# Performance work log

Measured on AMD Instinct MI355X. Metric: run time of the kernel, lower is better.

The kernel has to match this reference:

```python
import jax, jax.numpy as jnp
import numpy as np

T, H, I, E = 2048, 2880, 2880, 8
TOP_K = 4
ALPHA = 1.702   # hidden_act_alpha
LIMIT = 7.0     # swiglu_limit
BETA = 1.0      # swiglu_beta


def setup_inputs() -> dict:
    key = jax.random.key(0)
    ks = jax.random.split(key, 10)
    s = 0.02
    return {
        "hidden_states": jax.random.normal(ks[0], (T, H), dtype=jnp.float32),
        "w_router": jax.random.normal(ks[1], (E, H), dtype=jnp.float32) * s,
        "b_router": jax.random.normal(ks[2], (E,), dtype=jnp.float32) * s,
        "w_gate": jax.random.normal(ks[3], (E, I, H), dtype=jnp.float32) * s,
        "b_gate": jax.random.normal(ks[4], (E, I), dtype=jnp.float32) * s,
        "w_up": jax.random.normal(ks[5], (E, I, H), dtype=jnp.float32) * s,
        "b_up": jax.random.normal(ks[6], (E, I), dtype=jnp.float32) * s,
        "w2": jax.random.normal(ks[7], (E, H, I), dtype=jnp.float32) * s,
        "b2": jax.random.normal(ks[8], (E, H), dtype=jnp.float32) * s,
        "num_global_tokens": T,
        "max_num_tokens_per_gpu": T,
    }


def reference(hidden_states, w_router, b_router, w_gate, b_gate, w_up, b_up,
              w2, b2, num_global_tokens, max_num_tokens_per_gpu):
    x = hidden_states  # [T, H]
    # ---- router + custom routing_function: topk then softmax over topk logits (fp32)
    router_logits = x @ w_router.T + b_router                 # [T, E]
    topk_vals, topk_idx = jax.lax.top_k(router_logits, TOP_K)  # [T, K]
    expert_weights = jax.nn.softmax(topk_vals.astype(jnp.float32), axis=-1)  # [T, K]
    # combine weights per expert: [T, E], nonzero only for the top-k experts
    tok = jnp.arange(x.shape[0])[:, None]
    combine = jnp.zeros((x.shape[0], E), dtype=jnp.float32).at[tok, topk_idx].add(expert_weights)
    # ---- experts: gpt-oss swiglu with clamp limits and +beta on up branch
    g = jnp.einsum('th,eih->tei', x, w_gate) + b_gate[None]   # [T, E, I]
    u = jnp.einsum('th,eih->tei', x, w_up) + b_up[None]       # [T, E, I]
    g = jnp.minimum(g, LIMIT)
    u = jnp.clip(u, -LIMIT, LIMIT)
    act = (u + BETA) * (g * jax.nn.sigmoid(ALPHA * g))        # [T, E, I]
    y = jnp.einsum('tei,ehi->teh', act, w2) + b2[None]        # [T, E, H]
    out = jnp.einsum('teh,te->th', y, combine)                # [T, H]
    return out.astype(x.dtype)
```

## Files before the change

### kernel.cpp

```cpp
#include <hip/hip_runtime.h>
#include <hip/hip_bf16.h>
#include <cstdint>

#define T_TOK 2048
#define HD    2880
#define ID    2880
#define NE    8
#define TOPK  4
#define ALPHA 1.702f
#define LIMIT 7.0f

typedef __attribute__((ext_vector_type(8))) short short8;
typedef __attribute__((ext_vector_type(4))) float floatx4;

__device__ __forceinline__ ushort f32_bf16(float f) {
    union { float f; uint32_t u; } c; c.f = f;
    uint32_t u = c.u;
    uint32_t r = (u + 0x7FFFu + ((u >> 16) & 1u)) >> 16;
    return (ushort)r;
}

__global__ __launch_bounds__(256) void cvt_x_kernel(const float* __restrict__ x,
                                                    ushort* __restrict__ xb) {
    int i = (blockIdx.x * 256 + threadIdx.x) * 4;
    float4 v = *(const float4*)(x + i);
    ushort4 o;
    o.x = f32_bf16(v.x); o.y = f32_bf16(v.y);
    o.z = f32_bf16(v.z); o.w = f32_bf16(v.w);
    *(ushort4*)(xb + i) = o;
}

__global__ __launch_bounds__(256) void router_kernel(
    const float* __restrict__ x, const float* __restrict__ wr,
    const float* __restrict__ br, int* __restrict__ cnt,
    int* __restrict__ tok_list, float* __restrict__ wgt_list) {
    const int t = blockIdx.x, tid = threadIdx.x;
    __shared__ float sx[HD];
    __shared__ float sred[NE][4];
    for (int h = tid; h < HD; h += 256) sx[h] = x[(size_t)t * HD + h];
    __syncthreads();
    float p[NE];
#pragma unroll
    for (int e = 0; e < NE; e++) p[e] = 0.f;
    for (int h = tid; h < HD; h += 256) {
        float xv = sx[h];
#pragma unroll
        for (int e = 0; e < NE; e++) p[e] = fmaf(xv, wr[e * HD + h], p[e]);
    }
#pragma unroll
    for (int e = 0; e < NE; e++) {
#pragma unroll
        for (int off = 32; off > 0; off >>= 1) p[e] += __shfl_down(p[e], off, 64);
    }
    if ((tid & 63) == 0) {
#pragma unroll
        for (int e = 0; e < NE; e++) sred[e][tid >> 6] = p[e];
    }
    __syncthreads();
    if (tid == 0) {
        float lg[NE];
#pragma unroll
        for (int e = 0; e < NE; e++)
            lg[e] = sred[e][0] + sred[e][1] + sred[e][2] + sred[e][3] + br[e];
        int idx[TOPK]; float val[TOPK];
        unsigned used = 0;
#pragma unroll
        for (int k = 0; k < TOPK; k++) {
            int best = -1; float bv = -1e30f;
#pragma unroll
            for (int e = 0; e < NE; e++) {
                if (!((used >> e) & 1u) && lg[e] > bv) { bv = lg[e]; best = e; }
            }
            used |= 1u << best; idx[k] = best; val[k] = bv;
        }
        float m = val[0];
        float ex[TOPK], s = 0.f;
#pragma unroll
        for (int k = 0; k < TOPK; k++) { ex[k] = __expf(val[k] - m); s += ex[k]; }
        float inv = 1.f / s;
#pragma unroll
        for (int k = 0; k < TOPK; k++) {
            int e = idx[k];
            int pos = atomicAdd(&cnt[e], 1);
            tok_list[e * T_TOK + pos] = t;
            wgt_list[e * T_TOK + pos] = ex[k] * inv;
        }
    }
}

__global__ void offsets_kernel(const int* __restrict__ cnt, int* __restrict__ ofs) {
    if (threadIdx.x == 0 && blockIdx.x == 0) {
        int s = 0;
        for (int e = 0; e < NE; e++) { ofs[e] = s; s += cnt[e]; }
    }
}

#define LDS_S 40
__global__ __launch_bounds__(256, 2) void expert_gu_kernel(
    const ushort* __restrict__ xb, const float* __restrict__ wg,
    const float* __restrict__ bg, const float* __restrict__ wu,
    const float* __restrict__ bu, const int* __restrict__ cnt,
    const int* __restrict__ ofs, const int* __restrict__ tok_list,
    ushort* __restrict__ act) {
    const int e = blockIdx.z;
    const int n_e = cnt[e];
    const int mBase = blockIdx.y * 128;
    if (mBase >= n_e) return;
    const int nBase = blockIdx.x * 128;
    const int tid = threadIdx.x;

    __shared__ ushort sA[128 * LDS_S];
    __shared__ ushort sBg[128 * LDS_S];
    __shared__ ushort sBu[128 * LDS_S];
    __shared__ int sTok[128];

    if (tid < 128) {
        int slot = mBase + tid;
        sTok[tid] = tok_list[e * T_TOK + (slot < n_e ? slot : 0)];
    }
    __syncthreads();

    const int wave = tid >> 6, lane = tid & 63;
    const int wm = (wave >> 1) * 64, wn = (wave & 1) * 64;
    const int ln = lane & 15, quad = lane >> 4;

    floatx4 accG[4][4], accU[4][4];
#pragma unroll
    for (int mi = 0; mi < 4; mi++)
#pragma unroll
        for (int ni = 0; ni < 4; ni++) {
            accG[mi][ni] = (floatx4){0.f, 0.f, 0.f, 0.f};
            accU[mi][ni] = (floatx4){0.f, 0.f, 0.f, 0.f};
        }

    const float* wgE = wg + (size_t)e * ID * HD;
    const float* wuE = wu + (size_t)e * ID * HD;

    for (int k0 = 0; k0 < HD; k0 += 32) {
#pragma unroll
        for (int r = 0; r < 2; r++) {
            int lin = r * 256 + tid;
            int ar = lin >> 2, ac = lin & 3;
            uint4 v = *(const uint4*)(xb + (size_t)sTok[ar] * HD + k0 + ac * 8);
            *(uint4*)&sA[ar * LDS_S + ac * 8] = v;
        }
#pragma unroll
        for (int r = 0; r < 4; r++) {
            int c = r * 256 + tid;
            int brow = c >> 3, bc = c & 7;
            int n = nBase + brow; if (n >= ID) n = ID - 1;
            float4 g4 = *(const float4*)(wgE + (size_t)n * HD + k0 + bc * 4);
            float4 u4 = *(const float4*)(wuE + (size_t)n * HD + k0 + bc * 4);
            ushort4 gg, uu;
            gg.x = f32_bf16(g4.x); gg.y = f32_bf16(g4.y);
            gg.z = f32_bf16(g4.z); gg.w = f32_bf16(g4.w);
            uu.x = f32_bf16(u4.x); uu.y = f32_bf16(u4.y);
            uu.z = f32_bf16(u4.z); uu.w = f32_bf16(u4.w);
            *(ushort4*)&sBg[brow * LDS_S + bc * 4] = gg;
            *(ushort4*)&sBu[brow * LDS_S + bc * 4] = uu;
        }
        __syncthreads();
        short8 af[4], bgf[4], buf_[4];
#pragma unroll
        for (int mi = 0; mi < 4; mi++)
            af[mi] = *(const short8*)&sA[(wm + mi * 16 + ln) * LDS_S + quad * 8];
#pragma unroll
        for (int ni = 0; ni < 4; ni++) {
            bgf[ni] = *(const short8*)&sBg[(wn + ni * 16 + ln) * LDS_S + quad * 8];
            buf_[ni] = *(const short8*)&sBu[(wn + ni * 16 + ln) * LDS_S + quad * 8];
        }
#pragma unroll
        for (int mi = 0; mi < 4; mi++)
#pragma unroll
            for (int ni = 0; ni < 4; ni++) {
                accG[mi][ni] = __builtin_amdgcn_mfma_f32_16x16x32_bf16(
                    af[mi], bgf[ni], accG[mi][ni], 0, 0, 0);
                accU[mi][ni] = __builtin_amdgcn_mfma_f32_16x16x32_bf16(
                    af[mi], buf_[ni], accU[mi][ni], 0, 0, 0);
            }
        __syncthreads();
    }

    const int row0 = ofs[e] + mBase;
#pragma unroll
    for (int mi = 0; mi < 4; mi++) {
#pragma unroll
        for (int r = 0; r < 4; r++) {
            int ml = wm + mi * 16 + quad * 4 + r;
            if (mBase + ml >= n_e) continue;
#pragma unroll
            for (int ni = 0; ni < 4; ni++) {
                int n = nBase + wn + ni * 16 + ln;
                if (n < ID) {
                    float g = accG[mi][ni][r] + bg[e * ID + n];
                    float u = accU[mi][ni][r] + bu[e * ID + n];
                    g = fminf(g, LIMIT);
                    u = fminf(fmaxf(u, -LIMIT), LIMIT);
                    float sg = 1.0f / (1.0f + __expf(-ALPHA * g));
                    float a = (u + 1.0f) * (g * sg);
                    act[(size_t)(row0 + ml) * ID + n] = f32_bf16(a);
                }
            }
        }
    }
}

__global__ __launch_bounds__(256, 2) void expert_down_kernel(
    const ushort* __restrict__ act, const float* __restrict__ w2,
    const float* __restrict__ b2, const int* __restrict__ cnt,
    const int* __restrict__ ofs, const int* __restrict__ tok_list,
    const float* __restrict__ wgt_list, float* __restrict__ out) {
    const int e = blockIdx.z;
    const int n_e = cnt[e];
    const int mBase = blockIdx.y * 128;
    if (mBase >= n_e) return;
    const int nBase = blockIdx.x * 128;
    const int tid = threadIdx.x;

    __shared__ ushort sA[128 * LDS_S];
    __shared__ ushort sB[128 * LDS_S];
    __shared__ int sTok[128];
    __shared__ float sWgt[128];

    if (tid < 128) {
        int slot = mBase + tid;
        int cs = (slot < n_e) ? slot : 0;
        sTok[tid] = tok_list[e * T_TOK + cs];
        sWgt[tid] = wgt_list[e * T_TOK + cs];
    }
    __syncthreads();

    const int wave = tid >> 6, lane = tid & 63;
    const int wm = (wave >> 1) * 64, wn = (wave & 1) * 64;
    const int ln = lane & 15, quad = lane >> 4;
    const int row0 = ofs[e] + mBase;

    floatx4 acc[4][4];
#pragma unroll
    for (int mi = 0; mi < 4; mi++)
#pragma unroll
        for (int ni = 0; ni < 4; ni++) acc[mi][ni] = (floatx4){0.f, 0.f, 0.f, 0.f};

    const float* w2E = w2 + (size_t)e * HD * ID;

    for (int k0 = 0; k0 < ID; k0 += 32) {
#pragma unroll
        for (int r = 0; r < 2; r++) {
            int lin = r * 256 + tid;
            int ar = lin >> 2, ac = lin & 3;
            int rr = (mBase + ar < n_e) ? ar : 0;
            uint4 v = *(const uint4*)(act + (size_t)(row0 + rr) * ID + k0 + ac * 8);
            *(uint4*)&sA[ar * LDS_S + ac * 8] = v;
        }
#pragma unroll
        for (int r = 0; r < 4; r++) {
            int c = r * 256 + tid;
            int brow = c >> 3, bc = c & 7;
            int n = nBase + brow; if (n >= HD) n = HD - 1;
            float4 b4 = *(const float4*)(w2E + (size_t)n * ID + k0 + bc * 4);
            ushort4 bb;
            bb.x = f32_bf16(b4.x); bb.y = f32_bf16(b4.y);
            bb.z = f32_bf16(b4.z); bb.w = f32_bf16(b4.w);
            *(ushort4*)&sB[brow * LDS_S + bc * 4] = bb;
        }
        __syncthreads();
        short8 af[4], bf[4];
#pragma unroll
        for (int mi = 0; mi < 4; mi++)
            af[mi] = *(const short8*)&sA[(wm + mi * 16 + ln) * LDS_S + quad * 8];
#pragma unroll
        for (int ni = 0; ni < 4; ni++)
            bf[ni] = *(const short8*)&sB[(wn + ni * 16 + ln) * LDS_S + quad * 8];
#pragma unroll
        for (int mi = 0; mi < 4; mi++)
#pragma unroll
            for (int ni = 0; ni < 4; ni++)
                acc[mi][ni] = __builtin_amdgcn_mfma_f32_16x16x32_bf16(
                    af[mi], bf[ni], acc[mi][ni], 0, 0, 0);
        __syncthreads();
    }

#pragma unroll
    for (int mi = 0; mi < 4; mi++) {
#pragma unroll
        for (int r = 0; r < 4; r++) {
            int ml = wm + mi * 16 + quad * 4 + r;
            if (mBase + ml >= n_e) continue;
            int token = sTok[ml];
            float wgt = sWgt[ml];
#pragma unroll
            for (int ni = 0; ni < 4; ni++) {
                int n = nBase + wn + ni * 16 + ln;
                if (n < HD) {
                    float v = (acc[mi][ni][r] + b2[e * HD + n]) * wgt;
                    atomicAdd(&out[(size_t)token * HD + n], v);
                }
            }
        }
    }
}

extern "C" void kernel_launch(void* const* d_in, const int* in_sizes, int n_in,
                              void* d_out, int out_size, void* d_ws, size_t ws_size,
                              hipStream_t stream) {
    const float* x  = (const float*)d_in[0];
    const float* wr = (const float*)d_in[1];
    const float* br = (const float*)d_in[2];
    const float* wg = (const float*)d_in[3];
    const float* bg = (const float*)d_in[4];
    const float* wu = (const float*)d_in[5];
    const float* bu = (const float*)d_in[6];
    const float* w2 = (const float*)d_in[7];
    const float* b2 = (const float*)d_in[8];
    float* out = (float*)d_out;

    char* ws = (char*)d_ws;
    int*    cnt      = (int*)ws;
    int*    ofs      = (int*)(ws + 256);
    int*    tok_list = (int*)(ws + 512);
    float*  wgt_list = (float*)(ws + 512 + 65536);
    ushort* xb       = (ushort*)(ws + 512 + 131072);
    ushort* act      = (ushort*)(ws + 512 + 131072 + 11796480);

    hipMemsetAsync(out, 0, (size_t)T_TOK * HD * sizeof(float), stream);
    hipMemsetAsync(cnt, 0, NE * sizeof(int), stream);

    cvt_x_kernel<<<(T_TOK * HD) / 4 / 256, 256, 0, stream>>>(x, xb);
    router_kernel<<<T_TOK, 256, 0, stream>>>(x, wr, br, cnt, tok_list, wgt_list);
    offsets_kernel<<<1, 64, 0, stream>>>(cnt, ofs);

    dim3 g1((ID + 127) / 128, T_TOK / 128, NE);
    expert_gu_kernel<<<g1, 256, 0, stream>>>(xb, wg, bg, wu, bu, cnt, ofs, tok_list, act);

    dim3 g2((HD + 127) / 128, T_TOK / 128, NE);
    expert_down_kernel<<<g2, 256, 0, stream>>>(act, w2, b2, cnt, ofs, tok_list, wgt_list, out);
}
```

Baseline: 1.847 ms.

## Pre-convert expert weights to bf16 and stream tiles via global_load_lds

```diff
diff --git a/kernel.cpp b/kernel.cpp
--- a/kernel.cpp
+++ b/kernel.cpp
@@ -1,6 +1,6 @@
 #include <hip/hip_runtime.h>
-#include <hip/hip_bf16.h>
 #include <cstdint>
+#include <cstddef>
 
 #define T_TOK 2048
 #define HD    2880
@@ -18,6 +18,13 @@
     uint32_t u = c.u;
     uint32_t r = (u + 0x7FFFu + ((u >> 16) & 1u)) >> 16;
     return (ushort)r;
+}
+
+__device__ __forceinline__ void gload_lds16(const void* g, void* l) {
+    __builtin_amdgcn_global_load_lds(
+        (const __attribute__((address_space(1))) void*)g,
+        (__attribute__((address_space(3))) void*)l,
+        16, 0, 0);
 }
 
 __global__ __launch_bounds__(256) void cvt_x_kernel(const float* __restrict__ x,
@@ -28,6 +35,18 @@
     o.x = f32_bf16(v.x); o.y = f32_bf16(v.y);
     o.z = f32_bf16(v.z); o.w = f32_bf16(v.w);
     *(ushort4*)(xb + i) = o;
+}
+
+__global__ __launch_bounds__(256) void cvt_w_kernel(const float* __restrict__ w,
+                                                    ushort* __restrict__ wb, int n4) {
+    int stride = gridDim.x * 256;
+    for (int i = blockIdx.x * 256 + threadIdx.x; i < n4; i += stride) {
+        float4 v = *(const float4*)(w + (size_t)i * 4);
+        ushort4 o;
+        o.x = f32_bf16(v.x); o.y = f32_bf16(v.y);
+        o.z = f32_bf16(v.z); o.w = f32_bf16(v.w);
+        *(ushort4*)(wb + (size_t)i * 4) = o;
+    }
 }
 
 __global__ __launch_bounds__(256) void router_kernel(
@@ -92,6 +111,208 @@
     if (threadIdx.x == 0 && blockIdx.x == 0) {
         int s = 0;
         for (int e = 0; e < NE; e++) { ofs[e] = s; s += cnt[e]; }
+    }
+}
+
+
+__global__ __launch_bounds__(256, 2) void expert_gu2_kernel(
+    const ushort* __restrict__ xb, const ushort* __restrict__ wgb,
+    const float* __restrict__ bg, const ushort* __restrict__ wub,
+    const float* __restrict__ bu, const int* __restrict__ cnt,
+    const int* __restrict__ ofs, const int* __restrict__ tok_list,
+    ushort* __restrict__ act) {
+    const int e = blockIdx.z;
+    const int n_e = cnt[e];
+    const int mBase = blockIdx.y * 128;
+    if (mBase >= n_e) return;
+    const int nBase = blockIdx.x * 128;
+    const int tid = threadIdx.x;
+
+    __shared__ __attribute__((aligned(16))) ushort sA[128 * 32];
+    __shared__ __attribute__((aligned(16))) ushort sBg[128 * 32];
+    __shared__ __attribute__((aligned(16))) ushort sBu[128 * 32];
+    __shared__ int sTok[128];
+
+    if (tid < 128) {
+        int slot = mBase + tid;
+        sTok[tid] = tok_list[e * T_TOK + (slot < n_e ? slot : 0)];
+    }
+    __syncthreads();
+
+    const ushort* wgE = wgb + (size_t)e * (size_t)ID * HD;
+    const ushort* wuE = wub + (size_t)e * (size_t)ID * HD;
+    const ushort* aSrc[2];
+    const ushort* gSrc[2];
+    const ushort* uSrc[2];
+#pragma unroll
+    for (int i = 0; i < 2; i++) {
+        int lin = i * 256 + tid;
+        int ar = lin >> 2, ac = lin & 3;
+        aSrc[i] = xb + (size_t)sTok[ar] * HD + ac * 8;
+        int n = nBase + ar; if (n >= ID) n = ID - 1;
+        gSrc[i] = wgE + (size_t)n * HD + ac * 8;
+        uSrc[i] = wuE + (size_t)n * HD + ac * 8;
+    }
+
+    const int wave = tid >> 6, lane = tid & 63;
+    const int wm = (wave >> 1) * 64, wn = (wave & 1) * 64;
+    const int ln = lane & 15, quad = lane >> 4;
+
+    floatx4 accG[4][4], accU[4][4];
+#pragma unroll
+    for (int mi = 0; mi < 4; mi++)
+#pragma unroll
+        for (int ni = 0; ni < 4; ni++) {
+            accG[mi][ni] = (floatx4){0.f, 0.f, 0.f, 0.f};
+            accU[mi][ni] = (floatx4){0.f, 0.f, 0.f, 0.f};
+        }
+
+    for (int k0 = 0; k0 < HD; k0 += 32) {
+#pragma unroll
+        for (int i = 0; i < 2; i++) {
+            int lin = i * 256 + tid;
+            gload_lds16(aSrc[i] + k0, &sA[lin * 8]);
+            gload_lds16(gSrc[i] + k0, &sBg[lin * 8]);
+            gload_lds16(uSrc[i] + k0, &sBu[lin * 8]);
+        }
+        __syncthreads();
+
+        short8 af[4], bgf[4], buf_[4];
+#pragma unroll
+        for (int mi = 0; mi < 4; mi++)
+            af[mi] = *(const short8*)&sA[(wm + mi * 16 + ln) * 32 + quad * 8];
+#pragma unroll
+        for (int ni = 0; ni < 4; ni++) {
+            bgf[ni] = *(const short8*)&sBg[(wn + ni * 16 + ln) * 32 + quad * 8];
+            buf_[ni] = *(const short8*)&sBu[(wn + ni * 16 + ln) * 32 + quad * 8];
+        }
+#pragma unroll
+        for (int mi = 0; mi < 4; mi++)
+#pragma unroll
+            for (int ni = 0; ni < 4; ni++) {
+                accG[mi][ni] = __builtin_amdgcn_mfma_f32_16x16x32_bf16(
+                    af[mi], bgf[ni], accG[mi][ni], 0, 0, 0);
+                accU[mi][ni] = __builtin_amdgcn_mfma_f32_16x16x32_bf16(
+                    af[mi], buf_[ni], accU[mi][ni], 0, 0, 0);
+            }
+        __syncthreads();
+    }
+
+    const int row0 = ofs[e] + mBase;
+#pragma unroll
+    for (int mi = 0; mi < 4; mi++) {
+#pragma unroll
+        for (int r = 0; r < 4; r++) {
+            int ml = wm + mi * 16 + quad * 4 + r;
+            if (mBase + ml >= n_e) continue;
+#pragma unroll
+            for (int ni = 0; ni < 4; ni++) {
+                int n = nBase + wn + ni * 16 + ln;
+                if (n < ID) {
+                    float g = accG[mi][ni][r] + bg[e * ID + n];
+                    float u = accU[mi][ni][r] + bu[e * ID + n];
+                    g = fminf(g, LIMIT);
+                    u = fminf(fmaxf(u, -LIMIT), LIMIT);
+                    float sg = 1.0f / (1.0f + __expf(-ALPHA * g));
+                    float a = (u + 1.0f) * (g * sg);
+                    act[(size_t)(row0 + ml) * ID + n] = f32_bf16(a);
+                }
+            }
+        }
+    }
+}
+
+__global__ __launch_bounds__(256, 2) void expert_down2_kernel(
+    const ushort* __restrict__ act, const ushort* __restrict__ w2b,
+    const float* __restrict__ b2, const int* __restrict__ cnt,
+    const int* __restrict__ ofs, const int* __restrict__ tok_list,
+    const float* __restrict__ wgt_list, float* __restrict__ out) {
+    const int e = blockIdx.z;
+    const int n_e = cnt[e];
+    const int mBase = blockIdx.y * 128;
+    if (mBase >= n_e) return;
+    const int nBase = blockIdx.x * 128;
+    const int tid = threadIdx.x;
+
+    __shared__ __attribute__((aligned(16))) ushort sA[128 * 32];
+    __shared__ __attribute__((aligned(16))) ushort sB[128 * 32];
+    __shared__ int sTok[128];
+    __shared__ float sWgt[128];
+
+    if (tid < 128) {
+        int slot = mBase + tid;
+        int cs = (slot < n_e) ? slot : 0;
+        sTok[tid] = tok_list[e * T_TOK + cs];
+        sWgt[tid] = wgt_list[e * T_TOK + cs];
+    }
+    __syncthreads();
+
+    const int row0 = ofs[e] + mBase;
+    const ushort* w2E = w2b + (size_t)e * (size_t)HD * ID;
+    const ushort* aSrc[2];
+    const ushort* bSrc[2];
+#pragma unroll
+    for (int i = 0; i < 2; i++) {
+        int lin = i * 256 + tid;
+        int ar = lin >> 2, ac = lin & 3;
+        int rr = (mBase + ar < n_e) ? ar : 0;
+        aSrc[i] = act + (size_t)(row0 + rr) * ID + ac * 8;
+        int n = nBase + ar; if (n >= HD) n = HD - 1;
+        bSrc[i] = w2E + (size_t)n * ID + ac * 8;
+    }
+
+    const int wave = tid >> 6, lane = tid & 63;
+    const int wm = (wave >> 1) * 64, wn = (wave & 1) * 64;
+    const int ln = lane & 15, quad = lane >> 4;
+
+    floatx4 acc[4][4];
+#pragma unroll
+    for (int mi = 0; mi < 4; mi++)
+#pragma unroll
+        for (int ni = 0; ni < 4; ni++) acc[mi][ni] = (floatx4){0.f, 0.f, 0.f, 0.f};
+
+    for (int k0 = 0; k0 < ID; k0 += 32) {
+#pragma unroll
+        for (int i = 0; i < 2; i++) {
+            int lin = i * 256 + tid;
+            gload_lds16(aSrc[i] + k0, &sA[lin * 8]);
+            gload_lds16(bSrc[i] + k0, &sB[lin * 8]);
+        }
+        __syncthreads();
+
+        short8 af[4], bf[4];
+#pragma unroll
+        for (int mi = 0; mi < 4; mi++)
+            af[mi] = *(const short8*)&sA[(wm + mi * 16 + ln) * 32 + quad * 8];
+#pragma unroll
+        for (int ni = 0; ni < 4; ni++)
+            bf[ni] = *(const short8*)&sB[(wn + ni * 16 + ln) * 32 + quad * 8];
+#pragma unroll
+        for (int mi = 0; mi < 4; mi++)
+#pragma unroll
+            for (int ni = 0; ni < 4; ni++)
+                acc[mi][ni] = __builtin_amdgcn_mfma_f32_16x16x32_bf16(
+                    af[mi], bf[ni], acc[mi][ni], 0, 0, 0);
+        __syncthreads();
+    }
+
+#pragma unroll
+    for (int mi = 0; mi < 4; mi++) {
+#pragma unroll
+        for (int r = 0; r < 4; r++) {
+            int ml = wm + mi * 16 + quad * 4 + r;
+            if (mBase + ml >= n_e) continue;
+            int token = sTok[ml];
+            float wgt = sWgt[ml];
+#pragma unroll
+            for (int ni = 0; ni < 4; ni++) {
+                int n = nBase + wn + ni * 16 + ln;
+                if (n < HD) {
+                    float v = (acc[mi][ni][r] + b2[e * HD + n]) * wgt;
+                    atomicAdd(&out[(size_t)token * HD + n], v);
+                }
+            }
+        }
     }
 }
 
@@ -319,8 +540,13 @@
     int*    ofs      = (int*)(ws + 256);
     int*    tok_list = (int*)(ws + 512);
     float*  wgt_list = (float*)(ws + 512 + 65536);
-    ushort* xb       = (ushort*)(ws + 512 + 131072);
-    ushort* act      = (ushort*)(ws + 512 + 131072 + 11796480);
+    ushort* xb       = (ushort*)(ws + 131584);
+    ushort* act      = (ushort*)(ws + 131584 + 11796480);
+    const size_t W_ELEMS = (size_t)NE * ID * HD;
+    ushort* wgb = (ushort*)(ws + 59113984);
+    ushort* wub = (ushort*)(ws + 59113984 + 132710400);
+    ushort* w2b = (ushort*)(ws + 59113984 + 2ull * 132710400);
+    const size_t NEED = 59113984ull + 3ull * 132710400ull;
 
     hipMemsetAsync(out, 0, (size_t)T_TOK * HD * sizeof(float), stream);
     hipMemsetAsync(cnt, 0, NE * sizeof(int), stream);
@@ -329,9 +555,24 @@
     router_kernel<<<T_TOK, 256, 0, stream>>>(x, wr, br, cnt, tok_list, wgt_list);
     offsets_kernel<<<1, 64, 0, stream>>>(cnt, ofs);
 
-    dim3 g1((ID + 127) / 128, T_TOK / 128, NE);
-    expert_gu_kernel<<<g1, 256, 0, stream>>>(xb, wg, bg, wu, bu, cnt, ofs, tok_list, act);
-
-    dim3 g2((HD + 127) / 128, T_TOK / 128, NE);
-    expert_down_kernel<<<g2, 256, 0, stream>>>(act, w2, b2, cnt, ofs, tok_list, wgt_list, out);
-}
+    if (ws_size >= NEED) {
+        const int n4 = (int)(W_ELEMS / 4);
+        cvt_w_kernel<<<8192, 256, 0, stream>>>(wg, wgb, n4);
+        cvt_w_kernel<<<8192, 256, 0, stream>>>(wu, wub, n4);
+        cvt_w_kernel<<<8192, 256, 0, stream>>>(w2, w2b, n4);
+
+        dim3 g1((ID + 127) / 128, T_TOK / 128, NE);
+        expert_gu2_kernel<<<g1, 256, 0, stream>>>(xb, wgb, bg, wub, bu, cnt, ofs,
+                                                  tok_list, act);
+        dim3 g2((HD + 127) / 128, T_TOK / 128, NE);
+        expert_down2_kernel<<<g2, 256, 0, stream>>>(act, w2b, b2, cnt, ofs, tok_list,
+                                                    wgt_list, out);
+    } else {
+        dim3 g1((ID + 127) / 128, T_TOK / 128, NE);
+        expert_gu_kernel<<<g1, 256, 0, stream>>>(xb, wg, bg, wu, bu, cnt, ofs,
+                                                 tok_list, act);
+        dim3 g2((HD + 127) / 128, T_TOK / 128, NE);
+        expert_down_kernel<<<g2, 256, 0, stream>>>(act, w2, b2, cnt, ofs, tok_list,
+                                                   wgt_list, out);
+    }
+}
```

Measured after the change: 1.723 ms. 1.07x faster.
